# Performance work log

Measured on AMD Instinct MI355X. Metric: run time of the kernel, lower is better.

## Reference

```python
import jax, jax.numpy as jnp
import numpy as np

BATCH, NUM_FRAMES, FFT_SIZE = 256, 256, 512

def setup_inputs() -> dict:
    key = jax.random.key(0)
    k1, k2 = jax.random.split(key)
    inputs = jax.random.normal(k1, (BATCH, NUM_FRAMES, FFT_SIZE), dtype=jnp.float32)
    # Hann-like window (cfg.win_fn is a fixed per-bin window of length fft_size)
    window_fn = (0.5 - 0.5 * jnp.cos(2.0 * jnp.pi * jnp.arange(FFT_SIZE, dtype=jnp.float32) / FFT_SIZE))
    return {"inputs": inputs, "window_fn": window_fn}

def reference(inputs, window_fn):
    # window each frame, FFT along last axis (norm='backward' is jnp default), keep real part
    spec = jnp.fft.fft(inputs * window_fn, axis=-1).real.astype(jnp.float32)
    # output shape (batch, num_frames, fft_size, 1) as in the original reshape
    return spec[..., None]
```

## Files before the change

kernel.cpp:

```cpp
#include <hip/hip_runtime.h>
#include <math.h>

#define FFT_N 512
#define LDS_STRIDE 576

#define WAVE_LDS_FENCE() do { \
    asm volatile("" ::: "memory"); \
    __builtin_amdgcn_wave_barrier(); \
    asm volatile("" ::: "memory"); \
} while (0)

__device__ __forceinline__ void fft8(float* re, float* im) {
    const float C = 0.70710678118654752440f;
    float tr[8], ti[8];
    tr[0]=re[0]+re[4]; ti[0]=im[0]+im[4];
    tr[4]=re[0]-re[4]; ti[4]=im[0]-im[4];
    tr[1]=re[1]+re[5]; ti[1]=im[1]+im[5];
    tr[5]=re[1]-re[5]; ti[5]=im[1]-im[5];
    tr[2]=re[2]+re[6]; ti[2]=im[2]+im[6];
    tr[6]=re[2]-re[6]; ti[6]=im[2]-im[6];
    tr[3]=re[3]+re[7]; ti[3]=im[3]+im[7];
    tr[7]=re[3]-re[7]; ti[7]=im[3]-im[7];
    { float a=tr[5], b=ti[5]; tr[5]=C*(a+b); ti[5]=C*(b-a); }
    { float a=tr[6], b=ti[6]; tr[6]=b;       ti[6]=-a;      }
    { float a=tr[7], b=ti[7]; tr[7]=C*(b-a); ti[7]=-C*(a+b);}
    {
        float s0r=tr[0]+tr[2], s0i=ti[0]+ti[2];
        float s2r=tr[0]-tr[2], s2i=ti[0]-ti[2];
        float s1r=tr[1]+tr[3], s1i=ti[1]+ti[3];
        float dr =tr[1]-tr[3], di =ti[1]-ti[3];
        float s3r= di, s3i=-dr;
        re[0]=s0r+s1r; im[0]=s0i+s1i;
        re[2]=s2r+s3r; im[2]=s2i+s3i;
        re[4]=s0r-s1r; im[4]=s0i-s1i;
        re[6]=s2r-s3r; im[6]=s2i-s3i;
    }
    {
        float s0r=tr[4]+tr[6], s0i=ti[4]+ti[6];
        float s2r=tr[4]-tr[6], s2i=ti[4]-ti[6];
        float s1r=tr[5]+tr[7], s1i=ti[5]+ti[7];
        float dr =tr[5]-tr[7], di =ti[5]-ti[7];
        float s3r= di, s3i=-dr;
        re[1]=s0r+s1r; im[1]=s0i+s1i;
        re[3]=s2r+s3r; im[3]=s2i+s3i;
        re[5]=s0r-s1r; im[5]=s0i-s1i;
        re[7]=s2r-s3r; im[7]=s2i-s3i;
    }
}

__device__ __forceinline__ void twiddle_chain(float* re, float* im,
                                              float c, float s) {
    float cr = c, ci = s;
#pragma unroll
    for (int k = 1; k < 8; ++k) {
        float a = re[k], b = im[k];
        re[k] = a * cr - b * ci;
        im[k] = a * ci + b * cr;
        float ncr = cr * c - ci * s;
        float nci = cr * s + ci * c;
        cr = ncr; ci = nci;
    }
}

__device__ __forceinline__ int swz3(int m) {
    return ((m ^ (m >> 2)) & 1)
         | (((m >> 3) & 7) << 1)
         | (((m >> 1) & 1) << 4)
         | (((m >> 2) & 1) << 5);
}

__global__ __launch_bounds__(64) void fft512_pack2_kernel(
        const float* __restrict__ x,
        const float* __restrict__ win,
        float* __restrict__ out) {
    __shared__ float2 L[LDS_STRIDE];

    const int lane = threadIdx.x & 63;
    const int pair = blockIdx.x;

    const int t4   = lane << 2;
    const int u    = lane & 15;
    const int pp   = lane >> 4;
    const int x0sw = (lane >> 2) & 3;
    const int l0r  = lane ^ pp;
    const int k1p  = lane >> 3;
    const int n3p  = lane & 7;
    const int rl   = (lane >> 3) | ((lane & 7) << 3);
    const int s3w  = swz3(rl);

    int sm[4], smm[4];
#pragma unroll
    for (int j = 0; j < 4; ++j) {
        const int m = 4 * u + j;
        sm[j]  = swz3(m);
        smm[j] = swz3((64 - m) & 63);
    }

    float cA, sA, cB, sB;
    __sincosf(-6.283185307179586f * (float)lane * (1.0f / 512.0f), &sA, &cA);
    __sincosf(-6.283185307179586f * (float)n3p  * (1.0f / 64.0f),  &sB, &cB);

    const float* __restrict__ x0 = x + (size_t)(2 * pair) * FFT_N;
    const float* __restrict__ x1 = x0 + FFT_N;

    const float4 w0  = *(const float4*)(win + t4);
    const float4 w1  = *(const float4*)(win + t4 + 256);
    const float4 xa0 = *(const float4*)(x0 + t4);
    const float4 xb0 = *(const float4*)(x1 + t4);
    const float4 xa1 = *(const float4*)(x0 + t4 + 256);
    const float4 xb1 = *(const float4*)(x1 + t4 + 256);

    {
        const float* a0 = (const float*)&xa0;
        const float* b0 = (const float*)&xb0;
        const float* a1 = (const float*)&xa1;
        const float* b1 = (const float*)&xb1;
        const float* W0 = (const float*)&w0;
        const float* W1 = (const float*)&w1;
#pragma unroll
        for (int j = 0; j < 4; ++j) {
            const int sl = j ^ x0sw;
            L[t4 +       sl] = make_float2(a0[j] * W0[j], b0[j] * W0[j]);
            L[t4 + 256 + sl] = make_float2(a1[j] * W1[j], b1[j] * W1[j]);
        }
    }
    WAVE_LDS_FENCE();

    float re[8], im[8];
#pragma unroll
    for (int n1 = 0; n1 < 8; ++n1) {
        float2 v = L[n1 * 64 + l0r];
        re[n1] = v.x; im[n1] = v.y;
    }
    WAVE_LDS_FENCE();

    fft8(re, im);
    twiddle_chain(re, im, cA, sA);

#pragma unroll
    for (int k1 = 0; k1 < 8; ++k1)
        L[k1 * 72 + lane] = make_float2(re[k1], im[k1]);
    WAVE_LDS_FENCE();
#pragma unroll
    for (int n2 = 0; n2 < 8; ++n2) {
        float2 v = L[k1p * 72 + n2 * 8 + n3p];
        re[n2] = v.x; im[n2] = v.y;
    }
    WAVE_LDS_FENCE();

    fft8(re, im);
    twiddle_chain(re, im, cB, sB);

#pragma unroll
    for (int k2 = 0; k2 < 8; ++k2)
        L[(k1p * 8 + k2) * 9 + n3p] = make_float2(re[k2], im[k2]);
    WAVE_LDS_FENCE();
#pragma unroll
    for (int n3 = 0; n3 < 8; ++n3) {
        float2 v = L[lane * 9 + n3];
        re[n3] = v.x; im[n3] = v.y;
    }
    WAVE_LDS_FENCE();

    fft8(re, im);

#pragma unroll
    for (int k3 = 0; k3 < 8; ++k3)
        L[(k3 << 6) + s3w] = make_float2(re[k3], im[k3]);
    WAVE_LDS_FENCE();

    float* __restrict__ o0 = out + (size_t)(2 * pair) * FFT_N;
    float* __restrict__ o1 = o0 + FFT_N;
#pragma unroll
    for (int half = 0; half < 2; ++half) {
        const int hk = 4 * half + pp;
        float4 ra, rb;
        float* pa = (float*)&ra;
        float* pb = (float*)&rb;
#pragma unroll
        for (int j = 0; j < 4; ++j) {
            const int m  = 4 * u + j;
            const int hn = ((512 - (hk << 6) - m) >> 6) & 7;
            const float2 zk = L[(hk << 6) + sm[j]];
            const float2 zn = L[(hn << 6) + smm[j]];
            pa[j] = 0.5f * (zk.x + zn.x);
            pb[j] = 0.5f * (zk.y + zn.y);
        }
        *(float4*)(o0 + 256 * half + t4) = ra;
        *(float4*)(o1 + 256 * half + t4) = rb;
    }
}

extern "C" void kernel_launch(void* const* d_in, const int* in_sizes, int n_in,
                              void* d_out, int out_size, void* d_ws, size_t ws_size,
                              hipStream_t stream) {
    const float* x   = (const float*)d_in[0];
    const float* win = (const float*)d_in[1];
    float* out       = (float*)d_out;

    const int rows  = in_sizes[0] / FFT_N;
    const int pairs = rows / 2;
    hipLaunchKernelGGL(fft512_pack2_kernel, dim3(pairs), dim3(64), 0, stream,
                       x, win, out);
}
```

Baseline: 229.4 us.

## Replace radix-8 FFT with fp16 MFMA DFT GEMM against windowed cosine matrix

Swaps the per-row LDS radix-8 FFT for a dense real DFT done as a GEMM. A prepass kernel builds a 512x512 fp16 matrix of window times cosine in the workspace, and a 128x128-tiled MFMA f16 GEMM multiplies the input rows by it, keeping only the real part. This moves the transform onto the matrix cores and drops the complex shuffles, at the price of O(N^2) arithmetic and fp16 rounding of inputs and weights, which may hurt accuracy. The old FFT path runs only when no workspace is provided.

```diff
diff --git a/kernel.cpp b/kernel.cpp
--- a/kernel.cpp
+++ b/kernel.cpp
@@ -2,6 +2,121 @@
 #include <math.h>
 
 #define FFT_N 512
+
+using half8 = __attribute__((ext_vector_type(8))) _Float16;
+using half4 = __attribute__((ext_vector_type(4))) _Float16;
+using f32x4 = __attribute__((ext_vector_type(4))) float;
+
+
+__global__ __launch_bounds__(128) void build_w_kernel(
+        const float* __restrict__ win, _Float16* __restrict__ W) {
+    const int f  = blockIdx.x;
+    const int t0 = threadIdx.x * 4;
+#pragma unroll
+    for (int j = 0; j < 4; ++j) {
+        const int t = t0 + j;
+        const int m = (t * f) & 511;
+        const float c = cosf((float)m * (6.283185307179586f / 512.0f));
+        W[f * 512 + t] = (_Float16)(win[t] * c);
+    }
+}
+
+#define BM 128
+#define BN 128
+#define BK 32
+
+__global__ __launch_bounds__(256) void dft_gemm_kernel(
+        const float* __restrict__ x,
+        const _Float16* __restrict__ W,
+        float* __restrict__ out) {
+    __shared__ _Float16 Ah[BM][BK + 8];
+    __shared__ _Float16 Bh[BN][BK + 8];
+
+    const int tid  = threadIdx.x;
+    const int lane = tid & 63;
+    const int w    = tid >> 6;
+    const int wm   = w >> 1;
+    const int wn   = w & 1;
+    const int l15  = lane & 15;
+    const int l4   = lane >> 4;
+
+    const int m_tile = (int)blockIdx.x >> 2;
+    const int n_tile = (int)blockIdx.x & 3;
+    const size_t bm = (size_t)m_tile * BM;
+    const int    bn = n_tile * BN;
+
+    const int arow = tid >> 3;
+    const int aseg = tid & 7;
+    const int brow = tid >> 1;
+    const int bseg = tid & 1;
+
+    f32x4 acc[4][4];
+#pragma unroll
+    for (int mi = 0; mi < 4; ++mi)
+#pragma unroll
+        for (int ni = 0; ni < 4; ++ni)
+            acc[mi][ni] = (f32x4){0.f, 0.f, 0.f, 0.f};
+
+    float4 areg[4];
+    float4 breg[2];
+
+#pragma unroll
+    for (int i = 0; i < 4; ++i)
+        areg[i] = *(const float4*)(x + (bm + arow + 32 * i) * 512 + aseg * 4);
+    breg[0] = *(const float4*)(W + (size_t)(bn + brow) * 512 + bseg * 8);
+    breg[1] = *(const float4*)(W + (size_t)(bn + brow) * 512 + (bseg + 2) * 8);
+
+    for (int s = 0; s < 16; ++s) {
+        __syncthreads();
+
+#pragma unroll
+        for (int i = 0; i < 4; ++i) {
+            half4 h;
+            h[0] = (_Float16)areg[i].x; h[1] = (_Float16)areg[i].y;
+            h[2] = (_Float16)areg[i].z; h[3] = (_Float16)areg[i].w;
+            *(half4*)&Ah[arow + 32 * i][aseg * 4] = h;
+        }
+        *(float4*)&Bh[brow][bseg * 8]       = breg[0];
+        *(float4*)&Bh[brow][(bseg + 2) * 8] = breg[1];
+
+        if (s + 1 < 16) {
+            const int k0 = (s + 1) * BK;
+#pragma unroll
+            for (int i = 0; i < 4; ++i)
+                areg[i] = *(const float4*)(x + (bm + arow + 32 * i) * 512 + k0 + aseg * 4);
+            breg[0] = *(const float4*)(W + (size_t)(bn + brow) * 512 + k0 + bseg * 8);
+            breg[1] = *(const float4*)(W + (size_t)(bn + brow) * 512 + k0 + (bseg + 2) * 8);
+        }
+        __syncthreads();
+
+        half8 af[4], bf[4];
+#pragma unroll
+        for (int mi = 0; mi < 4; ++mi)
+            af[mi] = *(half8*)&Ah[wm * 64 + mi * 16 + l15][l4 * 8];
+#pragma unroll
+        for (int ni = 0; ni < 4; ++ni)
+            bf[ni] = *(half8*)&Bh[wn * 64 + ni * 16 + l15][l4 * 8];
+#pragma unroll
+        for (int mi = 0; mi < 4; ++mi)
+#pragma unroll
+            for (int ni = 0; ni < 4; ++ni)
+                acc[mi][ni] = __builtin_amdgcn_mfma_f32_16x16x32_f16(
+                    af[mi], bf[ni], acc[mi][ni], 0, 0, 0);
+    }
+
+#pragma unroll
+    for (int mi = 0; mi < 4; ++mi) {
+        const size_t r0 = bm + wm * 64 + mi * 16 + l4 * 4;
+#pragma unroll
+        for (int q = 0; q < 4; ++q) {
+            float* orow = out + (r0 + q) * 512 + bn + wn * 64 + l15;
+#pragma unroll
+            for (int ni = 0; ni < 4; ++ni)
+                orow[ni * 16] = acc[mi][ni][q];
+        }
+    }
+}
+
 #define LDS_STRIDE 576
 
 #define WAVE_LDS_FENCE() do { \
@@ -74,10 +189,8 @@
         const float* __restrict__ win,
         float* __restrict__ out) {
     __shared__ float2 L[LDS_STRIDE];
-
     const int lane = threadIdx.x & 63;
     const int pair = blockIdx.x;
-
     const int t4   = lane << 2;
     const int u    = lane & 15;
     const int pp   = lane >> 4;
@@ -87,7 +200,6 @@
     const int n3p  = lane & 7;
     const int rl   = (lane >> 3) | ((lane & 7) << 3);
     const int s3w  = swz3(rl);
-
     int sm[4], smm[4];
 #pragma unroll
     for (int j = 0; j < 4; ++j) {
@@ -95,21 +207,17 @@
         sm[j]  = swz3(m);
         smm[j] = swz3((64 - m) & 63);
     }
-
     float cA, sA, cB, sB;
     __sincosf(-6.283185307179586f * (float)lane * (1.0f / 512.0f), &sA, &cA);
     __sincosf(-6.283185307179586f * (float)n3p  * (1.0f / 64.0f),  &sB, &cB);
-
     const float* __restrict__ x0 = x + (size_t)(2 * pair) * FFT_N;
     const float* __restrict__ x1 = x0 + FFT_N;
-
     const float4 w0  = *(const float4*)(win + t4);
     const float4 w1  = *(const float4*)(win + t4 + 256);
     const float4 xa0 = *(const float4*)(x0 + t4);
     const float4 xb0 = *(const float4*)(x1 + t4);
     const float4 xa1 = *(const float4*)(x0 + t4 + 256);
     const float4 xb1 = *(const float4*)(x1 + t4 + 256);
-
     {
         const float* a0 = (const float*)&xa0;
         const float* b0 = (const float*)&xb0;
@@ -125,7 +233,6 @@
         }
     }
     WAVE_LDS_FENCE();
-
     float re[8], im[8];
 #pragma unroll
     for (int n1 = 0; n1 < 8; ++n1) {
@@ -133,10 +240,8 @@
         re[n1] = v.x; im[n1] = v.y;
     }
     WAVE_LDS_FENCE();
-
     fft8(re, im);
     twiddle_chain(re, im, cA, sA);
-
 #pragma unroll
     for (int k1 = 0; k1 < 8; ++k1)
         L[k1 * 72 + lane] = make_float2(re[k1], im[k1]);
@@ -147,10 +252,8 @@
         re[n2] = v.x; im[n2] = v.y;
     }
     WAVE_LDS_FENCE();
-
     fft8(re, im);
     twiddle_chain(re, im, cB, sB);
-
 #pragma unroll
     for (int k2 = 0; k2 < 8; ++k2)
         L[(k1p * 8 + k2) * 9 + n3p] = make_float2(re[k2], im[k2]);
@@ -161,14 +264,11 @@
         re[n3] = v.x; im[n3] = v.y;
     }
     WAVE_LDS_FENCE();
-
     fft8(re, im);
-
 #pragma unroll
     for (int k3 = 0; k3 < 8; ++k3)
         L[(k3 << 6) + s3w] = make_float2(re[k3], im[k3]);
     WAVE_LDS_FENCE();
-
     float* __restrict__ o0 = out + (size_t)(2 * pair) * FFT_N;
     float* __restrict__ o1 = o0 + FFT_N;
 #pragma unroll
@@ -197,9 +297,18 @@
     const float* x   = (const float*)d_in[0];
     const float* win = (const float*)d_in[1];
     float* out       = (float*)d_out;
-
-    const int rows  = in_sizes[0] / FFT_N;
-    const int pairs = rows / 2;
-    hipLaunchKernelGGL(fft512_pack2_kernel, dim3(pairs), dim3(64), 0, stream,
-                       x, win, out);
-}
+    const int rows   = in_sizes[0] / FFT_N;
+
+    if (d_ws != nullptr && ws_size >= (size_t)512 * 512 * sizeof(_Float16)) {
+        _Float16* W = (_Float16*)d_ws;
+        hipLaunchKernelGGL(build_w_kernel, dim3(512), dim3(128), 0, stream,
+                           win, W);
+        const int blocks = (rows / BM) * (512 / BN);
+        hipLaunchKernelGGL(dft_gemm_kernel, dim3(blocks), dim3(256), 0, stream,
+                           x, W, out);
+    } else {
+        const int pairs = rows / 2;
+        hipLaunchKernelGGL(fft512_pack2_kernel, dim3(pairs), dim3(64), 0, stream,
+                           x, win, out);
+    }
+}
```

New measurement: 315.0 us. +37.3%, slower.
